# Optimization experiments

Hardware: AMD Instinct MI355X
Metric: run time of the kernel (lower is better)

## Reference

```python
import jax, jax.numpy as jnp
import numpy as np

NEG = -1e18


def _split_heads(x, h):
    # [B, L, D] -> [B, H, L, D/H]
    b, l, d = x.shape
    return x.reshape(b, l, h, d // h).transpose(0, 2, 1, 3)


def _merge_heads(x):
    # [B, H, L, Dh] -> [B, L, H*Dh]
    b, h, l, dh = x.shape
    return x.transpose(0, 2, 1, 3).reshape(b, l, h * dh)


def _sparse(att, dp_map):
    # att: [B, H, L] per-token scores; dp_map: [B, 2, L] (row, col) tree indices.
    # scatter att[b,h,t] -> S[b, h, dp_map[b,0,t], dp_map[b,1,t]], then symmetrize.
    B, H, L = att.shape
    bi = jnp.arange(B)[:, None, None]          # [B,1,1]
    hi = jnp.arange(H)[None, :, None]          # [1,H,1]
    p0 = dp_map[:, 0, :][:, None, :]           # [B,1,L]
    p1 = dp_map[:, 1, :][:, None, :]           # [B,1,L]
    s = jnp.zeros((B, H, L, L), att.dtype)
    s = s.at[bi, hi, p0, p1].set(att)          # matches torch index_put_ (overwrite)
    return s + jnp.swapaxes(s, 2, 3)


def _reverse(values, dp_map):
    # r[b, j] = values[b, dp_map[b,0,j]] for j >= 1; r[b,0] = 0
    idx = dp_map[:, 0, :]                      # [B, L]
    r = jnp.take_along_axis(values, idx[:, :, None], axis=1)
    return r.at[:, 0, :].set(0.0)


def setup_inputs() -> dict:
    key = jax.random.key(0)
    ks = jax.random.split(key, 16)
    B, L, D, R, H = 16, 384, 768, 768, 12
    inp = {
        "queries":   jax.random.normal(ks[0], (B, L, D), jnp.float32),
        "keys":      jax.random.normal(ks[1], (B, L, D), jnp.float32),
        "values":    jax.random.normal(ks[2], (B, L, D), jnp.float32),
        "relations": jax.random.normal(ks[3], (B, L, R), jnp.float32),
        "dp_map":    jax.random.randint(ks[4], (B, 2, L), 0, L, jnp.int32),
        "mask":      jax.random.bernoulli(ks[5], 0.1, (B, L, L)),
        "rel_mask":  jax.random.bernoulli(ks[6], 0.1, (B, L, 1)),
        "Wq":  jax.random.normal(ks[7],  (D, D), jnp.float32) * 0.02,
        "Wk":  jax.random.normal(ks[8],  (D, D), jnp.float32) * 0.02,
        "Wv":  jax.random.normal(ks[9],  (D, D), jnp.float32) * 0.02,
        "Wo":  jax.random.normal(ks[10], (D, D), jnp.float32) * 0.02,
        "Wge": jax.random.normal(ks[11], (D, R), jnp.float32) * 0.02,
        "Wgr": jax.random.normal(ks[12], (R, R), jnp.float32) * 0.02,
        "Vr":  jax.random.normal(ks[13], (R, 1), jnp.float32) * 0.02,
        "Vg":  jax.random.normal(ks[14], (R, 1), jnp.float32) * 0.02,
    }
    return inp


def reference(queries, keys, values, relations, dp_map, mask, rel_mask,
              Wq, Wk, Wv, Wo, Wge, Wgr, Vr, Vg):
    H = 12
    R = Vg.shape[0]
    Dk = Wq.shape[1]
    scale = (Dk // H) ** -0.5

    # config.is_reverse = True path
    hv = jnp.where(rel_mask, 0.0, _reverse(values, dp_map))       # [B,L,D]
    rel = jnp.where(rel_mask, 0.0, relations)                     # [B,L,R]

    # semantic gated mechanism
    rv_h = _split_heads(rel @ Wgr, H)                             # [B,H,L,R/H]
    hs_h = _split_heads(hv @ Wge, H)
    Vg_h = Vg.reshape(H, R // H, 1)
    g = jnp.tanh(jnp.einsum('bhld,hdo->bhlo', hs_h + rv_h, Vg_h))[..., 0]
    gated = _sparse(g, dp_map)                                    # [B,H,L,L]

    q = _split_heads(queries @ Wq, H) * scale
    k = _split_heads(keys @ Wk, H)
    v = _split_heads(values @ Wv, H)
    rel_h = _split_heads(rel, H)
    Vr_h = Vr.reshape(H, R // H, 1)

    self_logits = jnp.einsum('bhqd,bhkd->bhqk', q, k)             # [B,H,L,L]
    rel_logits = _sparse(jnp.einsum('bhld,hdo->bhlo', rel_h, Vr_h)[..., 0], dp_map)

    m = mask[:, None]                                             # [B,1,L,L]
    self_logits = jnp.where(m, NEG, self_logits)
    rel_logits = jnp.where(m, NEG, rel_logits)

    attention_weights = self_logits.sum(axis=1) / H               # [B,L,L]
    sw = jax.nn.softmax(self_logits, axis=-1)
    rw = jax.nn.softmax(rel_logits, axis=-1)
    w = (1.0 - gated) * sw + gated * rw                           # dropout p=0

    ctx = jnp.einsum('bhqk,bhkd->bhqd', w, v)
    out = _merge_heads(ctx) @ Wo
    return out, attention_weights
```

## Files before the change

### kernel.cpp

```cpp
#include <hip/hip_runtime.h>
#include <math.h>

#define Bn 16
#define Lq 384
#define Hn 12
#define Dm 768
#define DH 64
#define QT2 16
#define NEGV (-1e18f)
#define SPADU 404
#define ECAP 32

typedef __attribute__((ext_vector_type(4))) float f32x4;
typedef __attribute__((ext_vector_type(8))) __bf16 bf16x8;
typedef __attribute__((ext_vector_type(4))) __bf16 bf16x4;
typedef unsigned short ushort_t;
typedef unsigned int uint_t;
typedef unsigned long long ull_t;

__device__ __forceinline__ ushort_t f2b(float f) {
  unsigned int u = __float_as_uint(f);
  unsigned int r = (u + 0x7FFFu + ((u >> 16) & 1u)) >> 16;
  return (ushort_t)r;
}
__device__ __forceinline__ float b2f(ushort_t u) {
  return __uint_as_float(((unsigned int)u) << 16);
}
__device__ __forceinline__ bf16x8 cvt8(float4 a, float4 b) {
  bf16x8 r;
  r[0] = (__bf16)a.x; r[1] = (__bf16)a.y; r[2] = (__bf16)a.z; r[3] = (__bf16)a.w;
  r[4] = (__bf16)b.x; r[5] = (__bf16)b.y; r[6] = (__bf16)b.z; r[7] = (__bf16)b.w;
  return r;
}

__global__ __launch_bounds__(256) void k_prep(
    const float* __restrict__ Wge, const float* __restrict__ Wgr,
    const float* __restrict__ Vg,
    float* __restrict__ Age, float* __restrict__ Agr,
    const float* __restrict__ W0, const float* __restrict__ W1,
    const float* __restrict__ W2, const float* __restrict__ W3,
    ushort_t* __restrict__ T0, ushort_t* __restrict__ T1,
    ushort_t* __restrict__ T2, ushort_t* __restrict__ T3,
    const int* __restrict__ dp, int* __restrict__ win,
    const int* __restrict__ mask, ull_t* __restrict__ mbits)
{
  __shared__ float vg[DH];
  __shared__ float t[32][33];
  int blk = blockIdx.x;
  if (blk < 24) {
    int which = blk / Hn;
    int h = blk % Hn;
    const float* Wsrc = which ? Wgr : Wge;
    float* dst = which ? Agr : Age;
    if (threadIdx.x < DH) vg[threadIdx.x] = Vg[h*DH + threadIdx.x];
    __syncthreads();
    for (int d = threadIdx.x; d < Dm; d += 256) {
      const float* wrow = Wsrc + (size_t)d*Dm + h*DH;
      float s = 0.f;
      #pragma unroll 8
      for (int j = 0; j < DH; ++j) s = fmaf(wrow[j], vg[j], s);
      dst[h*Dm + d] = s;
    }
  } else if (blk < 24 + 2304) {
    int b2 = blk - 24;
    int z = b2 / 576, rem = b2 % 576;
    const float* W = (z == 0) ? W0 : (z == 1) ? W1 : (z == 2) ? W2 : W3;
    ushort_t* WT = (z == 0) ? T0 : (z == 1) ? T1 : (z == 2) ? T2 : T3;
    int k0 = (rem / 24)*32, n0 = (rem % 24)*32;
    int tx = threadIdx.x & 31, ty = threadIdx.x >> 5;
    #pragma unroll
    for (int r = 0; r < 4; ++r)
      t[ty + r*8][tx] = W[(size_t)(k0 + ty + r*8)*Dm + n0 + tx];
    __syncthreads();
    #pragma unroll
    for (int r = 0; r < 4; ++r)
      WT[(size_t)(n0 + ty + r*8)*Dm + k0 + tx] = f2b(t[tx][ty + r*8]);
  } else if (blk < 2352) {
    int i = (blk - 2328)*256 + threadIdx.x;
    int b = i / Lq, l = i % Lq;
    int p0 = dp[(size_t)(b*2+0)*Lq + l];
    int p1 = dp[(size_t)(b*2+1)*Lq + l];
    atomicMax(&win[(size_t)b*Lq*Lq + (size_t)p0*Lq + p1], l);
  } else {
    int rr = blk - 2352;
    int lane = threadIdx.x & 63, wave = threadIdx.x >> 6;
    int gi = rr*4 + wave;
    const int* mrow = mask + (size_t)gi*Lq;
    ull_t w0 = __ballot(mrow[lane]        != 0);
    ull_t w1 = __ballot(mrow[lane + 64]   != 0);
    ull_t w2 = __ballot(mrow[lane + 128]  != 0);
    ull_t w3 = __ballot(mrow[lane + 192]  != 0);
    ull_t w4 = __ballot(mrow[lane + 256]  != 0);
    ull_t w5 = __ballot(mrow[lane + 320]  != 0);
    if (lane == 0) {
      ull_t* out = mbits + (size_t)gi*6;
      out[0] = w0; out[1] = w1; out[2] = w2;
      out[3] = w3; out[4] = w4; out[5] = w5;
    }
  }
}

__global__ __launch_bounds__(256) void k_collect(
    const int* __restrict__ win, uint_t* __restrict__ ent,
    int* __restrict__ rowcnt)
{
  __shared__ int tB[32][33];
  int b = blockIdx.z;
  int i0 = blockIdx.x*32, j0 = blockIdx.y*32;
  const int* wb = win + (size_t)b*Lq*Lq;
  int tx = threadIdx.x & 31, ty = threadIdx.x >> 5;
  #pragma unroll
  for (int rr = 0; rr < 4; ++rr) {
    int r = ty + rr*8;
    tB[r][tx] = wb[(size_t)(j0+r)*Lq + i0 + tx];
  }
  __syncthreads();
  #pragma unroll
  for (int rr = 0; rr < 4; ++rr) {
    int ti = ty + rr*8;
    int i = i0 + ti, j = j0 + tx;
    int l1 = wb[(size_t)i*Lq + j];
    int l2 = tB[tx][ti];
    if (l1 >= 0 || l2 >= 0) {
      int slot = atomicAdd(&rowcnt[(size_t)b*Lq + i], 1);
      if (slot < ECAP)
        ent[((size_t)b*Lq + i)*ECAP + slot] =
            (uint_t)j | ((uint_t)(l1 + 1) << 9) | ((uint_t)(l2 + 1) << 19);
    }
  }
}

__global__ __launch_bounds__(256) void k_grlog(
    const float* __restrict__ values, const float* __restrict__ relations,
    const int* __restrict__ dp, const int* __restrict__ rel_mask,
    const float* __restrict__ Age, const float* __restrict__ Agr,
    const float* __restrict__ Vr,
    float* __restrict__ g, float* __restrict__ rlog)
{
  int blk = blockIdx.x;
  int b = blk / (Lq/4), l0 = (blk % (Lq/4))*4;
  int tid = threadIdx.x, lane = tid & 63, wave = tid >> 6;
  __shared__ float relrow[4][Dm], hvrow[4][Dm];
  #pragma unroll
  for (int rr = 0; rr < 4; ++rr) {
    int l = l0 + rr;
    int rm = rel_mask[(size_t)b*Lq + l];
    int idx = dp[(size_t)(b*2)*Lq + l];
    const float* vrow = values + ((size_t)b*Lq + idx)*Dm;
    const float* rrow = relations + ((size_t)b*Lq + l)*Dm;
    for (int d = tid; d < Dm; d += 256) {
      relrow[rr][d] = rm ? 0.f : rrow[d];
      hvrow[rr][d]  = (rm || l == 0) ? 0.f : vrow[d];
    }
  }
  __syncthreads();
  int l = l0 + wave;
  for (int h = 0; h < Hn; ++h) {
    float p = 0.f;
    #pragma unroll
    for (int k = 0; k < Dm/64; ++k) {
      int d = lane + 64*k;
      p = fmaf(hvrow[wave][d], Age[h*Dm + d],
          fmaf(relrow[wave][d], Agr[h*Dm + d], p));
    }
    #pragma unroll
    for (int o = 32; o > 0; o >>= 1) p += __shfl_xor(p, o);
    if (lane == 0) g[((size_t)b*Hn + h)*Lq + l] = tanhf(p);
  }
  if (lane < Hn) {
    float s = 0.f;
    #pragma unroll 8
    for (int j = 0; j < DH; ++j)
      s = fmaf(relrow[wave][lane*DH + j], Vr[lane*DH + j], s);
    rlog[((size_t)b*Hn + lane)*Lq + l] = s;
  }
}

__global__ __launch_bounds__(256) void k_mmqkv(
    const float* __restrict__ Xq, const float* __restrict__ Xk,
    const float* __restrict__ Xv,
    const ushort_t* __restrict__ WqT, const ushort_t* __restrict__ WkT,
    const ushort_t* __restrict__ WvT,
    ushort_t* __restrict__ qbf, ushort_t* __restrict__ kbf,
    ushort_t* __restrict__ vTbf)
{
  const int K = Dm;
  __shared__ ushort_t As[128*64];
  __shared__ ushort_t Bs[128*64];

  int z = blockIdx.z;
  const float* A     = (z == 0) ? Xq : (z == 1) ? Xk : Xv;
  const ushort_t* BT = (z == 0) ? WqT : (z == 1) ? WkT : WvT;

  int bm = blockIdx.x;
  int bn = blockIdx.y;
  int m_blk = bm*128;

  int t = threadIdx.x;
  int wave = t >> 6, lane = t & 63;
  int wr = wave >> 1, wc = wave & 1;
  int lrow = lane & 15, lkg = lane >> 4;

  f32x4 acc[4][4];
  #pragma unroll
  for (int i = 0; i < 4; ++i)
    #pragma unroll
    for (int j = 0; j < 4; ++j) acc[i][j] = (f32x4)(0.f);

  int sr = t >> 3, sc8 = t & 7;
  for (int k0 = 0; k0 < K; k0 += 64) {
    __syncthreads();
    #pragma unroll
    for (int i = 0; i < 4; ++i) {
      int row = sr + i*32;
      const float* ap = A + (size_t)(m_blk + row)*K + k0 + sc8*8;
      float4 f0 = *(const float4*)ap;
      float4 f1 = *(const float4*)(ap + 4);
      uint4 vb = *(const uint4*)(BT + (size_t)(bn*128 + row)*K + k0 + sc8*8);
      int slot = sc8 ^ (row & 7);
      *(bf16x8*)&As[row*64 + slot*8] = cvt8(f0, f1);
      *(uint4*)&Bs[row*64 + slot*8] = vb;
    }
    __syncthreads();
    #pragma unroll
    for (int kk = 0; kk < 2; ++kk) {
      bf16x8 aF[4], bF[4];
      int chunk = kk*4 + lkg;
      #pragma unroll
      for (int mi = 0; mi < 4; ++mi) {
        int arow = wr*64 + mi*16 + lrow;
        aF[mi] = *(const bf16x8*)&As[arow*64 + ((chunk ^ (arow & 7)) << 3)];
        int brow = wc*64 + mi*16 + lrow;
        bF[mi] = *(const bf16x8*)&Bs[brow*64 + ((chunk ^ (brow & 7)) << 3)];
      }
      #pragma unroll
      for (int mi = 0; mi < 4; ++mi)
        #pragma unroll
        for (int ni = 0; ni < 4; ++ni)
          acc[mi][ni] = __builtin_amdgcn_mfma_f32_16x16x32_bf16(
              aF[mi], bF[ni], acc[mi][ni], 0, 0, 0);
    }
  }

  float alpha = (z == 0) ? 0.125f : 1.f;
  #pragma unroll
  for (int mi = 0; mi < 4; ++mi) {
    #pragma unroll
    for (int ni = 0; ni < 4; ++ni) {
      f32x4 a = acc[mi][ni];
      int rit = wr*64 + mi*16 + 4*lkg;
      int cit = wc*64 + ni*16 + lrow;
      int gcol = bn*128 + cit;
      if (z < 2) {
        ushort_t* Cb = z ? kbf : qbf;
        int grow = m_blk + rit;
        #pragma unroll
        for (int r = 0; r < 4; ++r)
          Cb[(size_t)(grow + r)*Dm + gcol] = f2b(a[r]*alpha);
      } else {
        int b = bm/3;
        int rl = (bm%3)*128 + rit;
        ushort4 u;
        u.x = f2b(a[0]); u.y = f2b(a[1]); u.z = f2b(a[2]); u.w = f2b(a[3]);
        *(ushort4*)&vTbf[((size_t)b*Dm + gcol)*Lq + rl] = u;
      }
    }
  }
}

template<int MODE>
__global__ __launch_bounds__(256) void k_mm64(
    const ushort_t* __restrict__ A, const ushort_t* __restrict__ BT,
    float* __restrict__ Cf, const int* __restrict__ mask, float alpha)
{
  const int K = Dm;
  __shared__ ushort_t As[64*64];
  __shared__ ushort_t Bs[128*64];

  int bm = blockIdx.x, bn = blockIdx.y, b = blockIdx.z;
  const ushort_t* Ab = (MODE == 3) ? A  + (size_t)b*Lq*Dm : A;
  const ushort_t* Bb = (MODE == 3) ? BT + (size_t)b*Lq*Dm : BT;
  int m0 = bm*64, n0 = bn*128;

  int t = threadIdx.x;
  int wave = t >> 6, lane = t & 63;
  int wr = wave >> 1, wc = wave & 1;
  int lrow = lane & 15, lkg = lane >> 4;

  f32x4 acc[2][4];
  #pragma unroll
  for (int i = 0; i < 2; ++i)
    #pragma unroll
    for (int j = 0; j < 4; ++j) acc[i][j] = (f32x4)(0.f);

  int sr = t >> 3, sc8 = t & 7;
  for (int k0 = 0; k0 < K; k0 += 64) {
    __syncthreads();
    #pragma unroll
    for (int i = 0; i < 2; ++i) {
      int row = sr + i*32;
      uint4 va = *(const uint4*)(Ab + (size_t)(m0 + row)*K + k0 + sc8*8);
      int slot = sc8 ^ (row & 7);
      *(uint4*)&As[row*64 + slot*8] = va;
    }
    #pragma unroll
    for (int i = 0; i < 4; ++i) {
      int row = sr + i*32;
      uint4 vb = *(const uint4*)(Bb + (size_t)(n0 + row)*K + k0 + sc8*8);
      int slot = sc8 ^ (row & 7);
      *(uint4*)&Bs[row*64 + slot*8] = vb;
    }
    __syncthreads();
    #pragma unroll
    for (int kk = 0; kk < 2; ++kk) {
      bf16x8 aF[2], bF[4];
      int chunk = kk*4 + lkg;
      #pragma unroll
      for (int mi = 0; mi < 2; ++mi) {
        int arow = wr*32 + mi*16 + lrow;
        aF[mi] = *(const bf16x8*)&As[arow*64 + ((chunk ^ (arow & 7)) << 3)];
      }
      #pragma unroll
      for (int ni = 0; ni < 4; ++ni) {
        int brow = wc*64 + ni*16 + lrow;
        bF[ni] = *(const bf16x8*)&Bs[brow*64 + ((chunk ^ (brow & 7)) << 3)];
      }
      #pragma unroll
      for (int mi = 0; mi < 2; ++mi)
        #pragma unroll
        for (int ni = 0; ni < 4; ++ni)
          acc[mi][ni] = __builtin_amdgcn_mfma_f32_16x16x32_bf16(
              aF[mi], bF[ni], acc[mi][ni], 0, 0, 0);
    }
  }

  #pragma unroll
  for (int mi = 0; mi < 2; ++mi) {
    #pragma unroll
    for (int ni = 0; ni < 4; ++ni) {
      f32x4 a = acc[mi][ni];
      int rit = wr*32 + mi*16 + 4*lkg;
      int cit = wc*64 + ni*16 + lrow;
      if (MODE == 0) {
        int grow = m0 + rit, gcol = n0 + cit;
        #pragma unroll
        for (int r = 0; r < 4; ++r)
          Cf[(size_t)(grow + r)*Dm + gcol] = a[r]*alpha;
      } else {
        int rl = m0 + rit, cl = n0 + cit;
        const int* mb2 = mask + (size_t)b*Lq*Lq;
        float* awb = Cf + (size_t)b*Lq*Lq;
        #pragma unroll
        for (int r = 0; r < 4; ++r) {
          int m = mb2[(size_t)(rl + r)*Lq + cl];
          awb[(size_t)(rl + r)*Lq + cl] = m ? NEGV : a[r]*alpha;
        }
      }
    }
  }
}

__global__ __launch_bounds__(256, 8) void k_attn3(
    const ushort_t* __restrict__ qbf, const ushort_t* __restrict__ kbf,
    const ushort_t* __restrict__ vT,
    const ull_t* __restrict__ mbits, const int* __restrict__ rowcnt,
    const uint_t* __restrict__ ent,
    const float* __restrict__ g, const float* __restrict__ rlog,
    ushort_t* __restrict__ ctxbf)
{
  __shared__ ushort_t S16[QT2][SPADU];
  __shared__ ull_t mb[QT2][6];
  __shared__ float2 rg2[Lq + 1];
  __shared__ uint_t entS[QT2*ECAP];
  __shared__ int cntS[QT2];

  int bid = blockIdx.x;
  int h  = bid % Hn;
  int qt = (bid / Hn) % (Lq/QT2);
  int b  = bid / (Hn * (Lq/QT2));
  int q0 = qt * QT2;
  int tid = threadIdx.x, lane = tid & 63, wave = tid >> 6;
  int lrow = lane & 15, lkg = lane >> 4;
  int w4 = wave*4;

  const float* gh = g    + ((size_t)b*Hn + h)*Lq;
  const float* rh = rlog + ((size_t)b*Hn + h)*Lq;

  if (tid < QT2*6) {
    int r = tid / 6, u = tid % 6;
    mb[r][u] = mbits[((size_t)b*Lq + q0 + r)*6 + u];
  }
  if (tid == 0) { rg2[0].x = 0.f; rg2[0].y = 0.f; }
  for (int e = tid; e < Lq; e += 256) {
    float2 v2; v2.x = rh[e]; v2.y = gh[e];
    rg2[e + 1] = v2;
  }
  #pragma unroll
  for (int e = tid; e < QT2*ECAP; e += 256)
    entS[e] = ent[((size_t)b*Lq + q0)*ECAP + e];
  if (tid < QT2) {
    int c = rowcnt[(size_t)b*Lq + q0 + tid];
    cntS[tid] = c > ECAP ? ECAP : c;
  }

  {
    const ushort_t* qb = qbf + ((size_t)b*Lq + q0 + lrow)*Dm + h*DH + lkg*8;
    bf16x8 aF0 = *(const bf16x8*)(qb);
    bf16x8 aF1 = *(const bf16x8*)(qb + 32);
    int col0 = wave*96;
    #pragma unroll
    for (int tt = 0; tt < 6; ++tt) {
      int col = col0 + tt*16 + lrow;
      const ushort_t* kb = kbf + ((size_t)b*Lq + col)*Dm + h*DH + lkg*8;
      bf16x8 bF0 = *(const bf16x8*)(kb);
      bf16x8 bF1 = *(const bf16x8*)(kb + 32);
      f32x4 z = (f32x4)(0.f);
      z = __builtin_amdgcn_mfma_f32_16x16x32_bf16(aF0, bF0, z, 0, 0, 0);
      z = __builtin_amdgcn_mfma_f32_16x16x32_bf16(aF1, bF1, z, 0, 0, 0);
      #pragma unroll
      for (int r = 0; r < 4; ++r)
        S16[4*lkg + r][col] = f2b(__expf(z[r]));
    }
  }
  __syncthreads();

  for (int r = 0; r < 4; ++r) {
    int row = w4 + r;
    ull_t mw[6];
    #pragma unroll
    for (int u = 0; u < 6; ++u) mw[u] = mb[row][u];
    float sv[6];
    float ssum = 0.f;
    #pragma unroll
    for (int u = 0; u < 6; ++u) {
      int kj = u*64 + lane;
      bool mk = (mw[u] >> lane) & 1ull;
      sv[u] = mk ? 0.f : b2f(S16[row][kj]);
      ssum += sv[u];
    }
    #pragma unroll
    for (int o = 32; o > 0; o >>= 1) ssum += __shfl_xor(ssum, o);
    int nun = 384;
    #pragma unroll
    for (int u = 0; u < 6; ++u) nun -= (int)__popcll(mw[u]);
    int cnt = cntS[row];
    const uint_t* erow = &entS[row*ECAP];
    float rext = 0.f;
    for (int e = 0; e < cnt; ++e) {
      uint_t en = erow[e];
      int j = en & 511;
      if ((mw[j >> 6] >> (j & 63)) & 1ull) continue;
      uint_t i1 = (en >> 9) & 1023;
      uint_t i2 = en >> 19;
      float rel = rg2[i1].x + rg2[i2].x;
      rext += __expf(rel) - 1.f;
    }
    float rsum = (float)nun + rext;
    float si = 1.f/ssum, ri = 1.f/rsum;
    ushort_t* prow = &S16[row][0];
    #pragma unroll
    for (int u = 0; u < 6; ++u)
      prow[u*64 + lane] = f2b(sv[u]*si);
    for (int e = 0; e < cnt; ++e) {
      uint_t en = erow[e];
      int j = en & 511;
      if ((mw[j >> 6] >> (j & 63)) & 1ull) continue;
      uint_t i1 = (en >> 9) & 1023;
      uint_t i2 = en >> 19;
      float rel = rg2[i1].x + rg2[i2].x;
      float gvv = rg2[i1].y + rg2[i2].y;
      float pfix = (1.f - gvv)*b2f(prow[j]) + gvv*__expf(rel)*ri;
      if (lane == 0) prow[j] = f2b(pfix);
    }
  }
  __syncthreads();

  {
    int dcol = h*DH + wave*16 + lrow;
    const ushort_t* vb = vT + ((size_t)b*Dm + dcol)*Lq + lkg*8;
    const ushort_t* prow = &S16[lrow][0];
    f32x4 o = (f32x4)(0.f);
    #pragma unroll
    for (int ks = 0; ks < 12; ++ks) {
      bf16x4 lo = *(const bf16x4*)(prow + ks*32 + lkg*8);
      bf16x4 hi = *(const bf16x4*)(prow + ks*32 + lkg*8 + 4);
      bf16x8 pa = __builtin_shufflevector(lo, hi, 0,1,2,3,4,5,6,7);
      bf16x8 bv = *(const bf16x8*)(vb + ks*32);
      o = __builtin_amdgcn_mfma_f32_16x16x32_bf16(pa, bv, o, 0, 0, 0);
    }
    #pragma unroll
    for (int r = 0; r < 4; ++r)
      ctxbf[((size_t)b*Lq + q0 + 4*lkg + r)*Dm + dcol] = f2b(o[r]);
  }
}

extern "C" void kernel_launch(void* const* d_in, const int* in_sizes, int n_in,
                              void* d_out, int out_size, void* d_ws, size_t ws_size,
                              hipStream_t stream) {
  const float* queries   = (const float*)d_in[0];
  const float* keys      = (const float*)d_in[1];
  const float* values    = (const float*)d_in[2];
  const float* relations = (const float*)d_in[3];
  const int*   dp_map    = (const int*)d_in[4];
  const int*   mask      = (const int*)d_in[5];
  const int*   rel_mask  = (const int*)d_in[6];
  const float* Wq  = (const float*)d_in[7];
  const float* Wk  = (const float*)d_in[8];
  const float* Wv  = (const float*)d_in[9];
  const float* Wo  = (const float*)d_in[10];
  const float* Wge = (const float*)d_in[11];
  const float* Wgr = (const float*)d_in[12];
  const float* Vr  = (const float*)d_in[13];
  const float* Vg  = (const float*)d_in[14];

  float* ws = (float*)d_ws;
  const size_t SZ   = (size_t)Bn*Lq*Dm;
  const size_t WINS = (size_t)Bn*Lq*Lq;
  const size_t GSZ  = (size_t)Bn*Hn*Lq;
  const size_t ROWS = (size_t)Bn*Lq;

  int*   win  = (int*)ws;
  float* g    = ws + WINS;
  float* rlog = g + GSZ;
  float* Age  = rlog + GSZ;
  float* Agr  = Age + (size_t)Hn*Dm;
  ull_t* mbits = (ull_t*)(Agr + (size_t)Hn*Dm);
  int*   rowcnt = (int*)(mbits + ROWS*6);
  uint_t* ent  = (uint_t*)(rowcnt + ROWS);
  ushort_t* p0 = (ushort_t*)(ent + ROWS*ECAP);
  ushort_t* qbf  = p0;
  ushort_t* kbf  = p0 + SZ;
  ushort_t* vTbf = p0 + 2*SZ;
  ushort_t* ctxbf= p0 + 3*SZ;
  ushort_t* WqT  = p0 + 4*SZ;
  ushort_t* WkT  = WqT + (size_t)Dm*Dm;
  ushort_t* WvT  = WkT + (size_t)Dm*Dm;
  ushort_t* WoT  = WvT + (size_t)Dm*Dm;

  float* outp = (float*)d_out;
  float* awp  = outp + SZ;

  hipMemsetAsync(win, 0xFF, WINS*sizeof(int), stream);
  hipMemsetAsync(rowcnt, 0, ROWS*sizeof(int), stream);
  k_prep<<<3888, 256, 0, stream>>>(Wge, Wgr, Vg, Age, Agr,
                                   Wq, Wk, Wv, Wo, WqT, WkT, WvT, WoT,
                                   dp_map, win, mask, mbits);
  k_grlog<<<Bn*Lq/4, 256, 0, stream>>>(values, relations, dp_map, rel_mask,
                                       Age, Agr, Vr, g, rlog);
  k_mmqkv<<<dim3(48, 6, 3), 256, 0, stream>>>(queries, keys, values,
                                              WqT, WkT, WvT, qbf, kbf, vTbf);
  k_collect<<<dim3(12, 12, Bn), 256, 0, stream>>>(win, ent, rowcnt);
  k_mm64<3><<<dim3(6, 3, Bn), 256, 0, stream>>>(qbf, kbf, awp, mask, 1.f/12.f);
  k_attn3<<<Bn*(Lq/QT2)*Hn, 256, 0, stream>>>(qbf, kbf, vTbf, mbits, rowcnt,
                                              ent, g, rlog, ctxbf);
  k_mm64<0><<<dim3(96, 6, 1), 256, 0, stream>>>(ctxbf, WoT, outp, nullptr, 1.f);
}
```

Before: 203.8 us.

## Fold masking and row sums into QK phase, defer softmax normalization to output

The attention kernel now applies the mask and accumulates per-row exp sums while writing scores after the QK MFMA. This removes the separate pass that reread and rewrote all 384 probabilities per row. The 1/sum normalization moves to the PV output, and the sparse relation fixups run in a single thread per row with a rescaled relation term. The bf16 conversion now uses the native cast. The change adds a barrier and serializes the fixup loop on 16 threads, and it stores unnormalized bf16 exponentials, which changes rounding.

```diff
diff --git a/kernel.cpp b/kernel.cpp
--- a/kernel.cpp
+++ b/kernel.cpp
@@ -19,9 +19,7 @@
 typedef unsigned long long ull_t;
 
 __device__ __forceinline__ ushort_t f2b(float f) {
-  unsigned int u = __float_as_uint(f);
-  unsigned int r = (u + 0x7FFFu + ((u >> 16) & 1u)) >> 16;
-  return (ushort_t)r;
+  return __builtin_bit_cast(ushort_t, (__bf16)f);
 }
 __device__ __forceinline__ float b2f(ushort_t u) {
   return __uint_as_float(((unsigned int)u) << 16);
@@ -373,6 +371,8 @@
   __shared__ float2 rg2[Lq + 1];
   __shared__ uint_t entS[QT2*ECAP];
   __shared__ int cntS[QT2];
+  __shared__ float pp[QT2][4];
+  __shared__ float sinvS[QT2];
 
   int bid = blockIdx.x;
   int h  = bid % Hn;
@@ -381,7 +381,6 @@
   int q0 = qt * QT2;
   int tid = threadIdx.x, lane = tid & 63, wave = tid >> 6;
   int lrow = lane & 15, lkg = lane >> 4;
-  int w4 = wave*4;
 
   const float* gh = g    + ((size_t)b*Hn + h)*Lq;
   const float* rh = rlog + ((size_t)b*Hn + h)*Lq;
@@ -402,75 +401,82 @@
     int c = rowcnt[(size_t)b*Lq + q0 + tid];
     cntS[tid] = c > ECAP ? ECAP : c;
   }
+  __syncthreads();
 
   {
     const ushort_t* qb = qbf + ((size_t)b*Lq + q0 + lrow)*Dm + h*DH + lkg*8;
     bf16x8 aF0 = *(const bf16x8*)(qb);
     bf16x8 aF1 = *(const bf16x8*)(qb + 32);
     int col0 = wave*96;
+    int w0 = col0 >> 6;
+    ull_t m0[4], m1[4];
+    #pragma unroll
+    for (int r = 0; r < 4; ++r) {
+      m0[r] = mb[4*lkg + r][w0];
+      m1[r] = mb[4*lkg + r][w0 + 1];
+    }
+    float ps[4] = {0.f, 0.f, 0.f, 0.f};
+    const ushort_t* kb = kbf + ((size_t)b*Lq + col0 + lrow)*Dm + h*DH + lkg*8;
     #pragma unroll
     for (int tt = 0; tt < 6; ++tt) {
       int col = col0 + tt*16 + lrow;
-      const ushort_t* kb = kbf + ((size_t)b*Lq + col)*Dm + h*DH + lkg*8;
       bf16x8 bF0 = *(const bf16x8*)(kb);
       bf16x8 bF1 = *(const bf16x8*)(kb + 32);
+      kb += 16*Dm;
       f32x4 z = (f32x4)(0.f);
       z = __builtin_amdgcn_mfma_f32_16x16x32_bf16(aF0, bF0, z, 0, 0, 0);
       z = __builtin_amdgcn_mfma_f32_16x16x32_bf16(aF1, bF1, z, 0, 0, 0);
-      #pragma unroll
-      for (int r = 0; r < 4; ++r)
-        S16[4*lkg + r][col] = f2b(__expf(z[r]));
+      bool hi = ((col0 + tt*16) >> 6) != w0;
+      int sh = col & 63;
+      #pragma unroll
+      for (int r = 0; r < 4; ++r) {
+        ull_t mw = hi ? m1[r] : m0[r];
+        bool mk = (mw >> sh) & 1ull;
+        float e = mk ? 0.f : __expf(z[r]);
+        ps[r] += e;
+        S16[4*lkg + r][col] = f2b(e);
+      }
+    }
+    #pragma unroll
+    for (int off = 1; off < 16; off <<= 1)
+      #pragma unroll
+      for (int r = 0; r < 4; ++r) ps[r] += __shfl_xor(ps[r], off);
+    if (lrow == 0) {
+      #pragma unroll
+      for (int r = 0; r < 4; ++r) pp[4*lkg + r][wave] = ps[r];
     }
   }
   __syncthreads();
 
-  for (int r = 0; r < 4; ++r) {
-    int row = w4 + r;
-    ull_t mw[6];
-    #pragma unroll
-    for (int u = 0; u < 6; ++u) mw[u] = mb[row][u];
-    float sv[6];
-    float ssum = 0.f;
-    #pragma unroll
-    for (int u = 0; u < 6; ++u) {
-      int kj = u*64 + lane;
-      bool mk = (mw[u] >> lane) & 1ull;
-      sv[u] = mk ? 0.f : b2f(S16[row][kj]);
-      ssum += sv[u];
-    }
-    #pragma unroll
-    for (int o = 32; o > 0; o >>= 1) ssum += __shfl_xor(ssum, o);
+  if (tid < QT2) {
+    int row = tid;
+    float ssum = pp[row][0] + pp[row][1] + pp[row][2] + pp[row][3];
+    float si = 1.f / ssum;
+    sinvS[row] = si;
     int nun = 384;
     #pragma unroll
-    for (int u = 0; u < 6; ++u) nun -= (int)__popcll(mw[u]);
+    for (int u = 0; u < 6; ++u) nun -= (int)__popcll(mb[row][u]);
     int cnt = cntS[row];
     const uint_t* erow = &entS[row*ECAP];
     float rext = 0.f;
     for (int e = 0; e < cnt; ++e) {
       uint_t en = erow[e];
       int j = en & 511;
-      if ((mw[j >> 6] >> (j & 63)) & 1ull) continue;
-      uint_t i1 = (en >> 9) & 1023;
-      uint_t i2 = en >> 19;
-      float rel = rg2[i1].x + rg2[i2].x;
+      if ((mb[row][j >> 6] >> (j & 63)) & 1ull) continue;
+      float rel = rg2[(en >> 9) & 1023].x + rg2[en >> 19].x;
       rext += __expf(rel) - 1.f;
     }
-    float rsum = (float)nun + rext;
-    float si = 1.f/ssum, ri = 1.f/rsum;
-    ushort_t* prow = &S16[row][0];
-    #pragma unroll
-    for (int u = 0; u < 6; ++u)
-      prow[u*64 + lane] = f2b(sv[u]*si);
+    float sr = ssum / ((float)nun + rext);
     for (int e = 0; e < cnt; ++e) {
       uint_t en = erow[e];
       int j = en & 511;
-      if ((mw[j >> 6] >> (j & 63)) & 1ull) continue;
-      uint_t i1 = (en >> 9) & 1023;
-      uint_t i2 = en >> 19;
-      float rel = rg2[i1].x + rg2[i2].x;
-      float gvv = rg2[i1].y + rg2[i2].y;
-      float pfix = (1.f - gvv)*b2f(prow[j]) + gvv*__expf(rel)*ri;
-      if (lane == 0) prow[j] = f2b(pfix);
+      if ((mb[row][j >> 6] >> (j & 63)) & 1ull) continue;
+      float2 a = rg2[(en >> 9) & 1023];
+      float2 c = rg2[en >> 19];
+      float er = __expf(a.x + c.x);
+      float gvv = a.y + c.y;
+      float ev = b2f(S16[row][j]);
+      S16[row][j] = f2b((1.f - gvv)*ev + gvv*er*sr);
     }
   }
   __syncthreads();
@@ -489,8 +495,10 @@
       o = __builtin_amdgcn_mfma_f32_16x16x32_bf16(pa, bv, o, 0, 0, 0);
     }
     #pragma unroll
-    for (int r = 0; r < 4; ++r)
-      ctxbf[((size_t)b*Lq + q0 + 4*lkg + r)*Dm + dcol] = f2b(o[r]);
+    for (int r = 0; r < 4; ++r) {
+      float si = sinvS[4*lkg + r];
+      ctxbf[((size_t)b*Lq + q0 + 4*lkg + r)*Dm + dcol] = f2b(o[r]*si);
+    }
   }
 }
 
```

Measured after the change: 200.5 us. Within noise of the previous version (-1.6%).
